# Performance work log

Measured on AMD Instinct MI355X. Metric: run time of the kernel, lower is better.

The kernel has to match this reference:

```python
import jax, jax.numpy as jnp
import numpy as np

B, T, HID = 1, 8192, 2048
NH, NKV, D = 32, 8, 64
BLK, LOCAL, GLOB = 64, 8, 1
THETA = 10000.0
SCALE = 1.0 / float(np.sqrt(D))
NEG = -1e9


def _sparse_tables(nb):
    """Replicates HumanVAttention._get_sparse_tables: per query block i select
    global blocks [0, GLOB) then local blocks [i-LOCAL+1, i], dedup keeping order."""
    max_sel = LOCAL + GLOB
    idx = np.zeros((nb, max_sel), np.int32)
    valid = np.zeros((nb, max_sel), bool)
    for i in range(nb):
        sel = [g for g in range(GLOB) if g < nb]
        sel += list(range(max(0, i - (LOCAL - 1)), i + 1))
        li, seen = [], set()
        for x in sel:
            if x not in seen:
                li.append(x); seen.add(x)
        idx[i, :len(li)] = li
        valid[i, :len(li)] = True
    return idx, valid


def _rotate_half(x):
    x1, x2 = x[..., : x.shape[-1] // 2], x[..., x.shape[-1] // 2:]
    return jnp.concatenate((-x2, x1), axis=-1)


def setup_inputs() -> dict:
    key = jax.random.key(0)
    ks = jax.random.split(key, 5)
    s = 0.02
    return {
        "hidden_states": jax.random.normal(ks[0], (B, T, HID), jnp.float32),
        "Wq": jax.random.normal(ks[1], (NH * D, HID), jnp.float32) * s,
        "Wk": jax.random.normal(ks[2], (NKV * D, HID), jnp.float32) * s,
        "Wv": jax.random.normal(ks[3], (NKV * D, HID), jnp.float32) * s,
        "Wo": jax.random.normal(ks[4], (NH * D, NH * D), jnp.float32) * s,
    }


def reference(hidden_states, Wq, Wk, Wv, Wo):
    hs = hidden_states
    # projections (nn.Linear: y = x @ W.T)
    q = (hs @ Wq.T).reshape(B, T, NH, D).transpose(0, 2, 1, 3)     # [B,NH,T,D]
    k = (hs @ Wk.T).reshape(B, T, NKV, D).transpose(0, 2, 1, 3)    # [B,NKV,T,D]
    v = (hs @ Wv.T).reshape(B, T, NKV, D).transpose(0, 2, 1, 3)

    # RoPE (full rotary factor)
    inv = 1.0 / (THETA ** (jnp.arange(0, D, 2, dtype=jnp.float32) / D))
    fr = jnp.arange(T, dtype=jnp.float32)[:, None] * inv[None, :]  # [T,D/2]
    emb = jnp.concatenate([fr, fr], axis=-1)                       # [T,D]
    cos = jnp.cos(emb)[None, None]                                 # [1,1,T,D]
    sin = jnp.sin(emb)[None, None]
    q = q * cos + _rotate_half(q) * sin
    k = k * cos + _rotate_half(k) * sin

    nb = T // BLK
    G = NH // NKV
    idx_np, valid_np = _sparse_tables(nb)
    max_sel = idx_np.shape[1]

    # gather selected K/V blocks per query block
    kb = k.reshape(B, NKV, nb, BLK, D)
    vb = v.reshape(B, NKV, nb, BLK, D)
    idx = jnp.asarray(idx_np)
    k_sel = kb[:, :, idx].reshape(B, NKV, nb, max_sel * BLK, D)    # [B,NKV,nb,M,D]
    v_sel = vb[:, :, idx].reshape(B, NKV, nb, max_sel * BLK, D)

    qg = q.reshape(B, NKV, G, nb, BLK, D)                          # grouped queries
    scores = jnp.einsum('bkgnqd,bknmd->bkgnqm',
                        qg.astype(jnp.float32), k_sel.astype(jnp.float32)) * SCALE

    # causal + validity mask over selected keys (static, built in numpy)
    kpos = (idx_np[:, :, None] * BLK + np.arange(BLK)).reshape(nb, -1)   # [nb,M]
    qpos = np.arange(nb)[:, None] * BLK + np.arange(BLK)                 # [nb,BLK]
    valid_flat = np.repeat(valid_np, BLK, axis=1)                        # [nb,M]
    allowed = valid_flat[:, None, :] & (kpos[:, None, :] <= qpos[:, :, None])
    scores = jnp.where(jnp.asarray(allowed)[None, None, None], scores, NEG)

    probs = jax.nn.softmax(scores, axis=-1)
    out = jnp.einsum('bkgnqm,bknmd->bkgnqd', probs.astype(v.dtype), v_sel)
    out = out.astype(hs.dtype).reshape(B, NH, T, D).transpose(0, 2, 1, 3)
    out = out.reshape(B, T, NH * D)
    return out @ Wo.T
```

## Files before the change

### kernel.cpp

```cpp
#include <hip/hip_runtime.h>
#include <cstdint>
#include <cstddef>

typedef __bf16 bf16;
typedef __attribute__((ext_vector_type(8))) __bf16 bf16x8;
typedef __attribute__((ext_vector_type(4))) __bf16 bf16x4;
typedef __attribute__((ext_vector_type(4))) float f32x4;

#define ATT_SCALE 0.125f
#define NEG_BIG  -1000000000.0f

__device__ __forceinline__ f32x4 mfma16(bf16x8 a, bf16x8 b, f32x4 c) {
  return __builtin_amdgcn_mfma_f32_16x16x32_bf16(a, b, c, 0, 0, 0);
}

__device__ __forceinline__ void gload16(const bf16* g, bf16* l) {
  __builtin_amdgcn_global_load_lds((__attribute__((address_space(1))) void*)g,
                                   (__attribute__((address_space(3))) void*)l,
                                   16, 0, 0);
}

__global__ __launch_bounds__(256) void prep_all(const float* __restrict__ hs,
                                                const float* __restrict__ Wq,
                                                const float* __restrict__ Wk,
                                                const float* __restrict__ Wv,
                                                const float* __restrict__ Wo,
                                                bf16* __restrict__ hs16, bf16* __restrict__ wq16,
                                                bf16* __restrict__ wk16, bf16* __restrict__ wv16,
                                                bf16* __restrict__ wo16,
                                                float* __restrict__ cosT, float* __restrict__ sinT) {
  int b = blockIdx.x, t = threadIdx.x;
  const float* src; bf16* dst; int i;
  if (b < 16384)      { src = hs; dst = hs16; i = b * 256 + t; }
  else if (b < 20480) { src = Wq; dst = wq16; i = (b - 16384) * 256 + t; }
  else if (b < 21504) { src = Wk; dst = wk16; i = (b - 20480) * 256 + t; }
  else if (b < 22528) { src = Wv; dst = wv16; i = (b - 21504) * 256 + t; }
  else if (b < 26624) { src = Wo; dst = wo16; i = (b - 22528) * 256 + t; }
  else {
    int idx = (b - 26624) * 256 + t;
    int tt = idx >> 5, j = idx & 31;
    float inv = exp2f(-(float)j * (13.287712379549449f / 32.0f));
    float fr = (float)tt * inv;
    cosT[idx] = cosf(fr); sinT[idx] = sinf(fr);
    return;
  }
  float4 v = *((const float4*)src + i);
  bf16x4 o;
  o[0] = (bf16)v.x; o[1] = (bf16)v.y; o[2] = (bf16)v.z; o[3] = (bf16)v.w;
  *((bf16x4*)dst + i) = o;
}

__global__ __launch_bounds__(512) void gemm_qkv(const bf16* __restrict__ A,
                                                const bf16* __restrict__ B0,
                                                const bf16* __restrict__ B1,
                                                const bf16* __restrict__ B2,
                                                bf16* __restrict__ C,
                                                const float* __restrict__ cosT,
                                                const float* __restrict__ sinT) {
  __shared__ bf16 As[3][8192];
  __shared__ bf16 Bs[3][12288];
  const int tid = threadIdx.x, lane = tid & 63, wid = tid >> 6;
  const int m0 = blockIdx.x * 256, n0 = blockIdx.y * 384;
  const int wr = wid >> 1, wc = wid & 1;
  const int fr = lane & 15, g4 = lane >> 4;
  const int sw8 = (g4 ^ ((fr >> 1) & 3)) * 8;

  f32x4 acc[4][12] = {};

  auto brow = [&](int n) -> const bf16* {
    if (n < 2048) return B0 + (size_t)n * 2048;
    if (n < 2560) return B1 + (size_t)(n - 2048) * 2048;
    return B2 + (size_t)(n - 2560) * 2048;
  };

  const int ra0 = tid >> 2, ra1 = 128 + (tid >> 2), rb2r = 256 + (tid >> 2);
  const bf16* aS0 = A + (size_t)(m0 + ra0) * 2048 + ((tid & 3) ^ ((ra0 >> 1) & 3)) * 8;
  const bf16* aS1 = A + (size_t)(m0 + ra1) * 2048 + ((tid & 3) ^ ((ra1 >> 1) & 3)) * 8;
  const bf16* bS0 = brow(n0 + ra0) + ((tid & 3) ^ ((ra0 >> 1) & 3)) * 8;
  const bf16* bS1 = brow(n0 + ra1) + ((tid & 3) ^ ((ra1 >> 1) & 3)) * 8;
  const bf16* bS2 = brow(n0 + rb2r) + ((tid & 3) ^ ((rb2r >> 1) & 3)) * 8;
  const int d0 = wid * 512, d1 = 4096 + wid * 512, d2 = 8192 + wid * 512;

#define STQA(BS, KT)  { bf16* d = &As[BS][0]; \
    gload16(aS0 + (KT) * 32, d + d0); gload16(aS1 + (KT) * 32, d + d1); }
#define STQB0(BS, KT) { bf16* d = &Bs[BS][0]; \
    gload16(bS0 + (KT) * 32, d + d0); gload16(bS1 + (KT) * 32, d + d1); }
#define STQB1(BS, KT) { gload16(bS2 + (KT) * 32, &Bs[BS][0] + d2); }

#define QTILE(KT, BI, BS, VM, STG) { \
    asm volatile("s_waitcnt vmcnt(" VM ")" ::: "memory"); \
    __builtin_amdgcn_s_barrier(); \
    __builtin_amdgcn_sched_barrier(0); \
    const bf16* Ab = &As[BI][0]; \
    const bf16* Bb = &Bs[BI][0]; \
    bf16x8 af[4], bfr[4]; \
    _Pragma("unroll") for (int mf = 0; mf < 4; ++mf) \
      af[mf] = *(const bf16x8*)(Ab + (wr * 64 + mf * 16 + fr) * 32 + sw8); \
    _Pragma("unroll") for (int q = 0; q < 4; ++q) \
      bfr[q] = *(const bf16x8*)(Bb + (wc * 192 + q * 16 + fr) * 32 + sw8); \
    if (STG) STQA(BS, (KT) + 2); \
    __builtin_amdgcn_s_setprio(1); \
    _Pragma("unroll") for (int mf = 0; mf < 4; ++mf) \
      _Pragma("unroll") for (int q = 0; q < 4; ++q) \
        acc[mf][q] = mfma16(af[mf], bfr[q], acc[mf][q]); \
    __builtin_amdgcn_s_setprio(0); \
    _Pragma("unroll") for (int q = 0; q < 4; ++q) \
      bfr[q] = *(const bf16x8*)(Bb + (wc * 192 + 64 + q * 16 + fr) * 32 + sw8); \
    if (STG) STQB0(BS, (KT) + 2); \
    __builtin_amdgcn_s_setprio(1); \
    _Pragma("unroll") for (int mf = 0; mf < 4; ++mf) \
      _Pragma("unroll") for (int q = 0; q < 4; ++q) \
        acc[mf][4 + q] = mfma16(af[mf], bfr[q], acc[mf][4 + q]); \
    __builtin_amdgcn_s_setprio(0); \
    _Pragma("unroll") for (int q = 0; q < 4; ++q) \
      bfr[q] = *(const bf16x8*)(Bb + (wc * 192 + 128 + q * 16 + fr) * 32 + sw8); \
    if (STG) STQB1(BS, (KT) + 2); \
    __builtin_amdgcn_s_setprio(1); \
    _Pragma("unroll") for (int mf = 0; mf < 4; ++mf) \
      _Pragma("unroll") for (int q = 0; q < 4; ++q) \
        acc[mf][8 + q] = mfma16(af[mf], bfr[q], acc[mf][8 + q]); \
    __builtin_amdgcn_s_setprio(0); \
  }

  STQA(0, 0); STQB0(0, 0); STQB1(0, 0);
  STQA(1, 1); STQB0(1, 1); STQB1(1, 1);

  int bi = 0, bs = 2;
  for (int kt = 0; kt < 62; ++kt) {
    QTILE(kt, bi, bs, "5", 1)
    bi = (bi == 2) ? 0 : bi + 1;
    bs = (bs == 2) ? 0 : bs + 1;
  }
  QTILE(62, bi, bs, "5", 0)
  bi = (bi == 2) ? 0 : bi + 1;
  QTILE(63, bi, bi, "0", 0)
#undef QTILE
#undef STQA
#undef STQB0
#undef STQB1

  const int fc = lane & 15, fr4 = (lane >> 4) * 4;
#pragma unroll
  for (int mf = 0; mf < 4; ++mf)
#pragma unroll
    for (int i = 0; i < 4; ++i) {
      size_t row = (size_t)(m0 + wr * 64 + mf * 16 + fr4 + i);
      bf16* base = C + row * 3072 + n0 + wc * 192;
      const float* cr = cosT + row * 32;
      const float* sr = sinT + row * 32;
#pragma unroll
      for (int g = 0; g < 3; ++g) {
        if (n0 + wc * 192 + g * 64 < 2560) {
#pragma unroll
          for (int q = 0; q < 2; ++q) {
            int j = q * 16 + fc;
            float c = cr[j], sn = sr[j];
            float x1 = acc[mf][g * 4 + q][i], x2 = acc[mf][g * 4 + q + 2][i];
            base[g * 64 + j]      = (bf16)(x1 * c - x2 * sn);
            base[g * 64 + j + 32] = (bf16)(x2 * c + x1 * sn);
          }
        } else {
#pragma unroll
          for (int q = 0; q < 4; ++q)
            base[g * 64 + q * 16 + fc] = (bf16)acc[mf][g * 4 + q][i];
        }
      }
    }
}

__global__ __launch_bounds__(512, 2) void gemm_out(const bf16* __restrict__ A,
                                                   const bf16* __restrict__ B0,
                                                   float* __restrict__ Cout) {
  __shared__ bf16 As[4][8192];
  __shared__ bf16 Bs[4][8192];
  const int tid = threadIdx.x, lane = tid & 63, wid = tid >> 6;
  const int m0 = blockIdx.x * 256, n0 = blockIdx.y * 256;
  const int wr = wid >> 2, wc = wid & 3;
  const int fr = lane & 15, g4 = lane >> 4;
  const int sw8 = (g4 ^ ((fr >> 1) & 3)) * 8;
  const int K = 2048, N = 2048;

  f32x4 acc[8][4] = {};

  const bf16* aS0; const bf16* aS1; const bf16* bS0; const bf16* bS1;
  {
    int c0 = tid, r0 = c0 >> 2, l0 = (c0 & 3) ^ ((r0 >> 1) & 3);
    int c1 = 512 + tid, r1 = c1 >> 2, l1 = (c1 & 3) ^ ((r1 >> 1) & 3);
    aS0 = A + (size_t)(m0 + r0) * K + l0 * 8;
    aS1 = A + (size_t)(m0 + r1) * K + l1 * 8;
    bS0 = B0 + (size_t)(n0 + r0) * K + l0 * 8;
    bS1 = B0 + (size_t)(n0 + r1) * K + l1 * 8;
  }
  const int dst0 = wid * 512;
  const int dst1 = 4096 + wid * 512;

#define STAGE_A(KT) { bf16* d = &As[(KT) & 3][0]; \
    gload16(aS0 + (KT) * 32, d + dst0); gload16(aS1 + (KT) * 32, d + dst1); }
#define STAGE_B(KT) { bf16* d = &Bs[(KT) & 3][0]; \
    gload16(bS0 + (KT) * 32, d + dst0); gload16(bS1 + (KT) * 32, d + dst1); }

#define KTILE(KT, VM, STG) { \
    asm volatile("s_waitcnt vmcnt(" VM ")" ::: "memory"); \
    __builtin_amdgcn_s_barrier(); \
    __builtin_amdgcn_sched_barrier(0); \
    const bf16* Ab = &As[(KT) & 3][0]; \
    const bf16* Bb = &Bs[(KT) & 3][0]; \
    bf16x8 bfr[4], af[4]; \
    _Pragma("unroll") for (int nf = 0; nf < 4; ++nf) \
      bfr[nf] = *(const bf16x8*)(Bb + (wc * 64 + nf * 16 + fr) * 32 + sw8); \
    _Pragma("unroll") for (int mf = 0; mf < 4; ++mf) \
      af[mf] = *(const bf16x8*)(Ab + (wr * 128 + mf * 16 + fr) * 32 + sw8); \
    if (STG) STAGE_A((KT) + 3); \
    __builtin_amdgcn_s_setprio(1); \
    _Pragma("unroll") for (int mf = 0; mf < 4; ++mf) \
      _Pragma("unroll") for (int nf = 0; nf < 4; ++nf) \
        acc[mf][nf] = mfma16(af[mf], bfr[nf], acc[mf][nf]); \
    __builtin_amdgcn_s_setprio(0); \
    _Pragma("unroll") for (int mf = 0; mf < 4; ++mf) \
      af[mf] = *(const bf16x8*)(Ab + (wr * 128 + 64 + mf * 16 + fr) * 32 + sw8); \
    if (STG) STAGE_B((KT) + 3); \
    __builtin_amdgcn_s_setprio(1); \
    _Pragma("unroll") for (int mf = 0; mf < 4; ++mf) \
      _Pragma("unroll") for (int nf = 0; nf < 4; ++nf) \
        acc[4 + mf][nf] = mfma16(af[mf], bfr[nf], acc[4 + mf][nf]); \
    __builtin_amdgcn_s_setprio(0); \
  }

  STAGE_A(0); STAGE_B(0);
  STAGE_A(1); STAGE_B(1);
  STAGE_A(2); STAGE_B(2);

  const int NT = K >> 5;
  for (int kt = 0; kt < NT - 3; ++kt) KTILE(kt, "8", 1)
  KTILE(NT - 3, "8", 0)
  KTILE(NT - 2, "4", 0)
  KTILE(NT - 1, "0", 0)
#undef KTILE
#undef STAGE_A
#undef STAGE_B

  const int fc = lane & 15, fr4 = (lane >> 4) * 4;
#pragma unroll
  for (int am = 0; am < 8; ++am)
#pragma unroll
    for (int i = 0; i < 4; ++i) {
      size_t row = (size_t)(m0 + wr * 128 + am * 16 + fr4 + i);
#pragma unroll
      for (int nf = 0; nf < 4; ++nf) {
        int col = n0 + wc * 64 + nf * 16 + fc;
        Cout[row * (size_t)N + col] = acc[am][nf][i];
      }
    }
}

__global__ __launch_bounds__(1024) void attn_sparse(const bf16* __restrict__ qkv,
                                                    bf16* __restrict__ attn) {
  const int iblk = blockIdx.x;
  const int kv = blockIdx.y;
  const int tid = threadIdx.x, lane = tid & 63, wid = tid >> 6;
  const int hloc = wid >> 2;
  const int h = kv * 4 + hloc;
  const int rg = wid & 3;

  __shared__ bf16 Ks[64 * 64];
  __shared__ bf16 Vt[2][64 * 72];
  __shared__ bf16 Ps[16 * 16 * 68];

  const int qcol = h * 64, kcol = 2048 + kv * 64, vcol = 2560 + kv * 64;
  const size_t trow0 = (size_t)iblk * 64;
  const int fr = lane & 15, g4 = lane >> 4, fk = g4 * 8, fr4 = g4 * 4;

  const bf16* qrow = qkv + (trow0 + rg * 16 + fr) * 3072 + qcol;
  bf16x8 bq0 = *(const bf16x8*)(qrow + fk);
  bf16x8 bq1 = *(const bf16x8*)(qrow + 32 + fk);

  float mrun = -INFINITY, lrun = 0.f;
  f32x4 acc[4] = {};

  const int kr = tid >> 3, ks = tid & 7;
  const int vu = tid & 511, vp = vu & 31, vd0 = (vu >> 5) * 4;
  const bool isK = (tid < 512);

  const int nsel = (iblk < 8) ? (iblk + 1) : 9;
  auto jof = [&](int js) { return (iblk < 8) ? js : ((js == 0) ? 0 : iblk - 8 + js); };

  {
    const size_t krow = (size_t)jof(0) * 64;
    if (isK) {
      const bf16* src = qkv + (krow + kr) * 3072 + kcol + ((ks ^ (kr & 7)) * 8);
      gload16(src, Ks + (tid >> 6) * 512);
    } else {
      const bf16* v0p = qkv + (krow + 2 * vp) * 3072 + vcol + vd0;
      uint64_t a = *(const uint64_t*)v0p;
      uint64_t b = *(const uint64_t*)(v0p + 3072);
#pragma unroll
      for (int e = 0; e < 4; ++e) {
        uint32_t w = (uint32_t)((a >> (16 * e)) & 0xFFFF) |
                     ((uint32_t)((b >> (16 * e)) & 0xFFFF) << 16);
        *(uint32_t*)(&Vt[0][0] + (vd0 + e) * 72 + 2 * vp) = w;
      }
    }
  }
  __syncthreads();

  for (int js = 0; js < nsel; ++js) {
    const int cur = js & 1;
    const int jblk = jof(js);
    const bool pre = (js + 1 < nsel);

    uint64_t va = 0, vb2 = 0;
    if (pre && !isK) {
      const bf16* v0p = qkv + ((size_t)jof(js + 1) * 64 + 2 * vp) * 3072 + vcol + vd0;
      va = *(const uint64_t*)v0p;
      vb2 = *(const uint64_t*)(v0p + 3072);
    }

    f32x4 s[4];
#pragma unroll
    for (int n = 0; n < 4; ++n) {
      const char* krowp = (const char*)Ks + (n * 16 + fr) * 128;
      bf16x8 kb0 = *(const bf16x8*)(krowp + ((g4 ^ (fr & 7)) << 4));
      bf16x8 kb1 = *(const bf16x8*)(krowp + (((4 + g4) ^ (fr & 7)) << 4));
      f32x4 z = {};
      z = mfma16(kb0, bq0, z);
      s[n] = mfma16(kb1, bq1, z);
    }

    __syncthreads();
    if (pre && isK) {
      const bf16* src = qkv + ((size_t)jof(js + 1) * 64 + kr) * 3072 + kcol +
                        ((ks ^ (kr & 7)) * 8);
      gload16(src, Ks + (tid >> 6) * 512);
    }

    const bool diag = (jblk == iblk);
    const int qr = rg * 16 + fr;
#pragma unroll
    for (int n = 0; n < 4; ++n)
#pragma unroll
      for (int i = 0; i < 4; ++i) {
        float sv = s[n][i] * ATT_SCALE;
        if (diag && (n * 16 + fr4 + i) > qr) sv = NEG_BIG;
        s[n][i] = sv;
      }

    float t0 = fmaxf(fmaxf(s[0][0], s[0][1]), fmaxf(s[0][2], s[0][3]));
    float t1 = fmaxf(fmaxf(s[1][0], s[1][1]), fmaxf(s[1][2], s[1][3]));
    float t2 = fmaxf(fmaxf(s[2][0], s[2][1]), fmaxf(s[2][2], s[2][3]));
    float t3 = fmaxf(fmaxf(s[3][0], s[3][1]), fmaxf(s[3][2], s[3][3]));
    float mx = fmaxf(fmaxf(t0, t1), fmaxf(t2, t3));
    mx = fmaxf(mx, __shfl_xor(mx, 16, 64));
    mx = fmaxf(mx, __shfl_xor(mx, 32, 64));
    float mnew = fmaxf(mrun, mx);
    float corr = __expf(mrun - mnew);
    mrun = mnew;
    float ps = 0.f;
#pragma unroll
    for (int n = 0; n < 4; ++n) {
      float p0 = __expf(s[n][0] - mnew), p1 = __expf(s[n][1] - mnew);
      float p2 = __expf(s[n][2] - mnew), p3 = __expf(s[n][3] - mnew);
      s[n][0] = p0; s[n][1] = p1; s[n][2] = p2; s[n][3] = p3;
      ps += (p0 + p1) + (p2 + p3);
    }
    ps += __shfl_xor(ps, 16, 64);
    ps += __shfl_xor(ps, 32, 64);
    lrun = lrun * corr + ps;

    float cq[4];
#pragma unroll
    for (int i = 0; i < 4; ++i) cq[i] = __shfl(corr, fr4 + i, 64);
#pragma unroll
    for (int n = 0; n < 4; ++n)
#pragma unroll
      for (int i = 0; i < 4; ++i) acc[n][i] *= cq[i];

    bf16* pbase = Ps + wid * (16 * 68);
#pragma unroll
    for (int n = 0; n < 4; ++n) {
      bf16x4 pk;
#pragma unroll
      for (int i = 0; i < 4; ++i) pk[i] = (bf16)s[n][i];
      *(bf16x4*)(pbase + fr * 68 + n * 16 + fr4) = pk;
    }
    bf16x8 pa0 = *(const bf16x8*)(pbase + fr * 68 + fk);
    bf16x8 pa1 = *(const bf16x8*)(pbase + fr * 68 + 32 + fk);

    if (pre && !isK) {
#pragma unroll
      for (int e = 0; e < 4; ++e) {
        uint32_t w = (uint32_t)((va >> (16 * e)) & 0xFFFF) |
                     ((uint32_t)((vb2 >> (16 * e)) & 0xFFFF) << 16);
        *(uint32_t*)(&Vt[cur ^ 1][0] + (vd0 + e) * 72 + 2 * vp) = w;
      }
    }

#pragma unroll
    for (int n = 0; n < 4; ++n) {
      bf16x8 vb0 = *(const bf16x8*)(&Vt[cur][0] + (n * 16 + fr) * 72 + fk);
      bf16x8 vb1 = *(const bf16x8*)(&Vt[cur][0] + (n * 16 + fr) * 72 + 32 + fk);
      acc[n] = mfma16(pa0, vb0, acc[n]);
      acc[n] = mfma16(pa1, vb1, acc[n]);
    }
    __syncthreads();
  }

  float lq[4];
#pragma unroll
  for (int i = 0; i < 4; ++i) lq[i] = __shfl(lrun, fr4 + i, 64);
#pragma unroll
  for (int i = 0; i < 4; ++i) {
    float rl = 1.0f / lq[i];
    size_t t = trow0 + rg * 16 + fr4 + i;
#pragma unroll
    for (int n = 0; n < 4; ++n)
      attn[t * 2048 + h * 64 + n * 16 + fr] = (bf16)(acc[n][i] * rl);
  }
}

extern "C" void kernel_launch(void* const* d_in, const int* in_sizes, int n_in,
                              void* d_out, int out_size, void* d_ws, size_t ws_size,
                              hipStream_t stream) {
  (void)in_sizes; (void)n_in; (void)out_size; (void)ws_size;
  const float* hs = (const float*)d_in[0];
  const float* Wq = (const float*)d_in[1];
  const float* Wk = (const float*)d_in[2];
  const float* Wv = (const float*)d_in[3];
  const float* Wo = (const float*)d_in[4];
  float* out = (float*)d_out;

  char* ws = (char*)d_ws;
  bf16* hs16 = (bf16*)(ws + 0);
  bf16* qkv  = (bf16*)(ws + 33554432);
  bf16* attn = (bf16*)(ws + 83886080);
  bf16* wq16 = (bf16*)(ws + 117440512);
  bf16* wk16 = (bf16*)(ws + 125829120);
  bf16* wv16 = (bf16*)(ws + 127926272);
  bf16* wo16 = (bf16*)(ws + 130023424);
  float* cosT = (float*)(ws + 138412032);
  float* sinT = (float*)(ws + 139460608);

  prep_all<<<27648, 256, 0, stream>>>(hs, Wq, Wk, Wv, Wo,
                                      hs16, wq16, wk16, wv16, wo16, cosT, sinT);

  gemm_qkv<<<dim3(32, 8), 512, 0, stream>>>(hs16, wq16, wk16, wv16, qkv, cosT, sinT);
  attn_sparse<<<dim3(128, 8), 1024, 0, stream>>>(qkv, attn);
  gemm_out<<<dim3(32, 8), 512, 0, stream>>>(attn, wo16, out);
}
```

Baseline: 299.6 us.

## Split attention blocks to two heads, double-buffer K, keep P in registers

Each attention workgroup now handles two query heads with 512 threads instead of four heads with 1024, which doubles the grid. Every thread loads both K (double-buffered in LDS, so one barrier per iteration is removed) and V. K rows are permuted on load so the QK^T output fragment can be packed straight into the PV MFMA A-operand, removing the LDS round-trip for P. The scale is folded into the exp via fma, the causal mask only runs on diagonal blocks, and setprio is raised around the MFMA sections; the cost is that K/V for each KV head are now loaded twice across workgroups.

```diff
diff --git a/kernel.cpp b/kernel.cpp
--- a/kernel.cpp
+++ b/kernel.cpp
@@ -8,7 +8,6 @@
 typedef __attribute__((ext_vector_type(4))) float f32x4;
 
 #define ATT_SCALE 0.125f
-#define NEG_BIG  -1000000000.0f
 
 __device__ __forceinline__ f32x4 mfma16(bf16x8 a, bf16x8 b, f32x4 c) {
   return __builtin_amdgcn_mfma_f32_16x16x32_bf16(a, b, c, 0, 0, 0);
@@ -253,18 +252,16 @@
     }
 }
 
-__global__ __launch_bounds__(1024) void attn_sparse(const bf16* __restrict__ qkv,
-                                                    bf16* __restrict__ attn) {
+__global__ __launch_bounds__(512) void attn_sparse(const bf16* __restrict__ qkv,
+                                                   bf16* __restrict__ attn) {
   const int iblk = blockIdx.x;
-  const int kv = blockIdx.y;
+  const int kv = blockIdx.y >> 1, pr = blockIdx.y & 1;
   const int tid = threadIdx.x, lane = tid & 63, wid = tid >> 6;
-  const int hloc = wid >> 2;
-  const int h = kv * 4 + hloc;
+  const int h = kv * 4 + pr * 2 + (wid >> 2);
   const int rg = wid & 3;
 
-  __shared__ bf16 Ks[64 * 64];
+  __shared__ bf16 Ks[2][64 * 64];
   __shared__ bf16 Vt[2][64 * 72];
-  __shared__ bf16 Ps[16 * 16 * 68];
 
   const int qcol = h * 64, kcol = 2048 + kv * 64, vcol = 2560 + kv * 64;
   const size_t trow0 = (size_t)iblk * 64;
@@ -278,27 +275,26 @@
   f32x4 acc[4] = {};
 
   const int kr = tid >> 3, ks = tid & 7;
-  const int vu = tid & 511, vp = vu & 31, vd0 = (vu >> 5) * 4;
-  const bool isK = (tid < 512);
+  const int pik = ((kr >> 5) << 5) + (((kr & 15) >> 2) << 3) + (((kr >> 4) & 1) << 2) + (kr & 3);
+  const int kso = ((ks ^ (kr & 7)) * 8);
+  const int vp = tid & 31, vd0 = (tid >> 5) * 4;
+
+  const int kb0m = fk, kb1m = fk + 4, kb2m = fk + 32, kb3m = fk + 36;
 
   const int nsel = (iblk < 8) ? (iblk + 1) : 9;
   auto jof = [&](int js) { return (iblk < 8) ? js : ((js == 0) ? 0 : iblk - 8 + js); };
 
   {
     const size_t krow = (size_t)jof(0) * 64;
-    if (isK) {
-      const bf16* src = qkv + (krow + kr) * 3072 + kcol + ((ks ^ (kr & 7)) * 8);
-      gload16(src, Ks + (tid >> 6) * 512);
-    } else {
-      const bf16* v0p = qkv + (krow + 2 * vp) * 3072 + vcol + vd0;
-      uint64_t a = *(const uint64_t*)v0p;
-      uint64_t b = *(const uint64_t*)(v0p + 3072);
-#pragma unroll
-      for (int e = 0; e < 4; ++e) {
-        uint32_t w = (uint32_t)((a >> (16 * e)) & 0xFFFF) |
-                     ((uint32_t)((b >> (16 * e)) & 0xFFFF) << 16);
-        *(uint32_t*)(&Vt[0][0] + (vd0 + e) * 72 + 2 * vp) = w;
-      }
+    gload16(qkv + (krow + pik) * 3072 + kcol + kso, &Ks[0][0] + (tid >> 6) * 512);
+    const bf16* v0p = qkv + (krow + 2 * vp) * 3072 + vcol + vd0;
+    uint64_t a = *(const uint64_t*)v0p;
+    uint64_t b = *(const uint64_t*)(v0p + 3072);
+#pragma unroll
+    for (int e = 0; e < 4; ++e) {
+      uint32_t w = (uint32_t)((a >> (16 * e)) & 0xFFFF) |
+                   ((uint32_t)((b >> (16 * e)) & 0xFFFF) << 16);
+      *(uint32_t*)(&Vt[0][0] + (vd0 + e) * 72 + 2 * vp) = w;
     }
   }
   __syncthreads();
@@ -307,42 +303,41 @@
     const int cur = js & 1;
     const int jblk = jof(js);
     const bool pre = (js + 1 < nsel);
+    const size_t nrow = pre ? (size_t)jof(js + 1) * 64 : 0;
 
     uint64_t va = 0, vb2 = 0;
-    if (pre && !isK) {
-      const bf16* v0p = qkv + ((size_t)jof(js + 1) * 64 + 2 * vp) * 3072 + vcol + vd0;
+    if (pre) {
+      const bf16* v0p = qkv + (nrow + 2 * vp) * 3072 + vcol + vd0;
       va = *(const uint64_t*)v0p;
       vb2 = *(const uint64_t*)(v0p + 3072);
     }
 
     f32x4 s[4];
+    __builtin_amdgcn_s_setprio(1);
 #pragma unroll
     for (int n = 0; n < 4; ++n) {
-      const char* krowp = (const char*)Ks + (n * 16 + fr) * 128;
-      bf16x8 kb0 = *(const bf16x8*)(krowp + ((g4 ^ (fr & 7)) << 4));
-      bf16x8 kb1 = *(const bf16x8*)(krowp + (((4 + g4) ^ (fr & 7)) << 4));
+      const char* krowp = (const char*)&Ks[cur][0] + (n * 16 + fr) * 128;
+      bf16x8 ka = *(const bf16x8*)(krowp + ((g4 ^ (fr & 7)) << 4));
+      bf16x8 kc = *(const bf16x8*)(krowp + (((4 + g4) ^ (fr & 7)) << 4));
       f32x4 z = {};
-      z = mfma16(kb0, bq0, z);
-      s[n] = mfma16(kb1, bq1, z);
-    }
-
-    __syncthreads();
-    if (pre && isK) {
-      const bf16* src = qkv + ((size_t)jof(js + 1) * 64 + kr) * 3072 + kcol +
-                        ((ks ^ (kr & 7)) * 8);
-      gload16(src, Ks + (tid >> 6) * 512);
-    }
-
-    const bool diag = (jblk == iblk);
-    const int qr = rg * 16 + fr;
-#pragma unroll
-    for (int n = 0; n < 4; ++n)
+      z = mfma16(ka, bq0, z);
+      s[n] = mfma16(kc, bq1, z);
+    }
+    __builtin_amdgcn_s_setprio(0);
+
+    if (pre)
+      gload16(qkv + (nrow + pik) * 3072 + kcol + kso, &Ks[cur ^ 1][0] + (tid >> 6) * 512);
+
+    if (jblk == iblk) {
+      const int qr = rg * 16 + fr;
 #pragma unroll
       for (int i = 0; i < 4; ++i) {
-        float sv = s[n][i] * ATT_SCALE;
-        if (diag && (n * 16 + fr4 + i) > qr) sv = NEG_BIG;
-        s[n][i] = sv;
+        if (kb0m + i > qr) s[0][i] = -1e30f;
+        if (kb1m + i > qr) s[1][i] = -1e30f;
+        if (kb2m + i > qr) s[2][i] = -1e30f;
+        if (kb3m + i > qr) s[3][i] = -1e30f;
       }
+    }
 
     float t0 = fmaxf(fmaxf(s[0][0], s[0][1]), fmaxf(s[0][2], s[0][3]));
     float t1 = fmaxf(fmaxf(s[1][0], s[1][1]), fmaxf(s[1][2], s[1][3]));
@@ -352,13 +347,16 @@
     mx = fmaxf(mx, __shfl_xor(mx, 16, 64));
     mx = fmaxf(mx, __shfl_xor(mx, 32, 64));
     float mnew = fmaxf(mrun, mx);
-    float corr = __expf(mrun - mnew);
+    float corr = __expf((mrun - mnew) * ATT_SCALE);
     mrun = mnew;
+    const float msc = mnew * ATT_SCALE;
     float ps = 0.f;
 #pragma unroll
     for (int n = 0; n < 4; ++n) {
-      float p0 = __expf(s[n][0] - mnew), p1 = __expf(s[n][1] - mnew);
-      float p2 = __expf(s[n][2] - mnew), p3 = __expf(s[n][3] - mnew);
+      float p0 = __expf(fmaf(s[n][0], ATT_SCALE, -msc));
+      float p1 = __expf(fmaf(s[n][1], ATT_SCALE, -msc));
+      float p2 = __expf(fmaf(s[n][2], ATT_SCALE, -msc));
+      float p3 = __expf(fmaf(s[n][3], ATT_SCALE, -msc));
       s[n][0] = p0; s[n][1] = p1; s[n][2] = p2; s[n][3] = p3;
       ps += (p0 + p1) + (p2 + p3);
     }
@@ -374,18 +372,16 @@
 #pragma unroll
       for (int i = 0; i < 4; ++i) acc[n][i] *= cq[i];
 
-    bf16* pbase = Ps + wid * (16 * 68);
-#pragma unroll
-    for (int n = 0; n < 4; ++n) {
-      bf16x4 pk;
-#pragma unroll
-      for (int i = 0; i < 4; ++i) pk[i] = (bf16)s[n][i];
-      *(bf16x4*)(pbase + fr * 68 + n * 16 + fr4) = pk;
-    }
-    bf16x8 pa0 = *(const bf16x8*)(pbase + fr * 68 + fk);
-    bf16x8 pa1 = *(const bf16x8*)(pbase + fr * 68 + 32 + fk);
-
-    if (pre && !isK) {
+    bf16x8 pa0, pa1;
+#pragma unroll
+    for (int i = 0; i < 4; ++i) {
+      pa0[i]     = (bf16)s[0][i];
+      pa0[4 + i] = (bf16)s[1][i];
+      pa1[i]     = (bf16)s[2][i];
+      pa1[4 + i] = (bf16)s[3][i];
+    }
+
+    if (pre) {
 #pragma unroll
       for (int e = 0; e < 4; ++e) {
         uint32_t w = (uint32_t)((va >> (16 * e)) & 0xFFFF) |
@@ -394,6 +390,7 @@
       }
     }
 
+    __builtin_amdgcn_s_setprio(1);
 #pragma unroll
     for (int n = 0; n < 4; ++n) {
       bf16x8 vb0 = *(const bf16x8*)(&Vt[cur][0] + (n * 16 + fr) * 72 + fk);
@@ -401,6 +398,8 @@
       acc[n] = mfma16(pa0, vb0, acc[n]);
       acc[n] = mfma16(pa1, vb1, acc[n]);
     }
+    __builtin_amdgcn_s_setprio(0);
+
     __syncthreads();
   }
 
@@ -443,6 +442,6 @@
                                       hs16, wq16, wk16, wv16, wo16, cosT, sinT);
 
   gemm_qkv<<<dim3(32, 8), 512, 0, stream>>>(hs16, wq16, wk16, wv16, qkv, cosT, sinT);
-  attn_sparse<<<dim3(128, 8), 1024, 0, stream>>>(qkv, attn);
+  attn_sparse<<<dim3(128, 16), 512, 0, stream>>>(qkv, attn);
   gemm_out<<<dim3(32, 8), 512, 0, stream>>>(attn, wo16, out);
 }
```

After: 267.6 us, median of 2. 1.12x faster.
